# Kernel tuning notes

Hardware: AMD Instinct MI355X
Metric: run time of the kernel (lower is better)

## Reference

```python
import jax, jax.numpy as jnp
import numpy as np

N_WIRES = 4
N_OPS = 20  # depth * 10
DIM = 2 ** N_WIRES

_CNOT4 = jnp.array([[1, 0, 0, 0],
                    [0, 1, 0, 0],
                    [0, 0, 0, 1],
                    [0, 0, 1, 0]], dtype=jnp.complex64)


def _ry(t):
    c, s = jnp.cos(t / 2), jnp.sin(t / 2)
    return jnp.stack([jnp.stack([c, -s], -1), jnp.stack([s, c], -1)], -2).astype(jnp.complex64)


def _rx(t):
    c = jnp.cos(t / 2).astype(jnp.complex64)
    s = (-1j) * jnp.sin(t / 2).astype(jnp.complex64)
    return jnp.stack([jnp.stack([c, s], -1), jnp.stack([s, c], -1)], -2)


def _rz(t):
    e = jnp.exp(-0.5j * t.astype(jnp.complex64))
    z = jnp.zeros_like(e)
    return jnp.stack([jnp.stack([e, z], -1), jnp.stack([z, jnp.conj(e)], -1)], -2)


def _apply_1q(state, U, w):
    # state: [B, 2^n]; U: [2,2] (shared) or [B,2,2] (per-batch angle)
    b = state.shape[0]
    left, right = 2 ** w, 2 ** (N_WIRES - w - 1)
    s = state.reshape(b, left, 2, right)
    if U.ndim == 2:
        s = jnp.einsum('ij,bajc->baic', U, s)
    else:
        s = jnp.einsum('bij,bajc->baic', U, s)
    return s.reshape(b, -1)


def _apply_cnot(state, c):
    # CNOT on adjacent wires (c, c+1)
    b = state.shape[0]
    left, right = 2 ** c, 2 ** (N_WIRES - c - 2)
    s = state.reshape(b, left, 4, right)
    s = jnp.einsum('ij,bajc->baic', _CNOT4, s)
    return s.reshape(b, -1)


def _circuit(x, y, theta):
    b = x.shape[0]
    state = jnp.zeros((b, DIM), jnp.complex64).at[:, 0].set(1.0)
    # encoder: Ry(x_w) on each wire
    for w in range(N_WIRES):
        state = _apply_1q(state, _ry(x[:, w]), w)
    # fixed pseudo-random layer of 20 gates (RX/RY/RZ rotations + CNOTs)
    rot = (_rx, _ry, _rz)
    for i in range(N_OPS):
        kind = i % 4
        if kind == 3:
            state = _apply_cnot(state, (i // 4) % (N_WIRES - 1))
        else:
            w = (7 * i + 3) % N_WIRES
            state = _apply_1q(state, rot[kind](theta[i]), w)
    # second encoder: Ry(-y_w)
    for w in range(N_WIRES):
        state = _apply_1q(state, _ry(-y[:, w]), w)
    # PauliZ expectation on wire 0, then abs (original: abs(measure(...)[0]))
    probs = state.real ** 2 + state.imag ** 2  # [B, 16]
    p = probs.reshape(b, 2, -1)
    z0 = jnp.sum(p[:, 0], -1) - jnp.sum(p[:, 1], -1)
    return jnp.abs(z0)


def setup_inputs() -> dict:
    key = jax.random.key(0)
    k1, k2, k3 = jax.random.split(key, 3)
    B = 262144
    x = jax.random.normal(k1, (B, N_WIRES), jnp.float32)
    y = jax.random.normal(k2, (B, N_WIRES), jnp.float32)
    theta = jax.random.normal(k3, (N_OPS,), jnp.float32)
    return {"x": x, "y": y, "theta": theta}


def reference(x, y, theta):
    return _circuit(x, y, theta)
```

## Files before the change

kernel.cpp:

```cpp
#include <hip/hip_runtime.h>
#include <hip/hip_bf16.h>
#include <math.h>


template<int BIT>
__device__ __forceinline__ void rx8(float (&sr)[8], float (&si)[8], float c, float s) {
    #pragma unroll
    for (int i = 0; i < 8; ++i) {
        if (!(i & (1 << BIT))) {
            const int j = i | (1 << BIT);
            float ar = sr[i], ai = si[i], br = sr[j], bi = si[j];
            sr[i] = c * ar + s * bi;  si[i] = c * ai - s * br;
            sr[j] = c * br + s * ai;  si[j] = c * bi - s * ar;
        }
    }
}

template<int BIT>
__device__ __forceinline__ void ry8(float (&sr)[8], float (&si)[8], float c, float s) {
    #pragma unroll
    for (int i = 0; i < 8; ++i) {
        if (!(i & (1 << BIT))) {
            const int j = i | (1 << BIT);
            float ar = sr[i], ai = si[i], br = sr[j], bi = si[j];
            sr[i] = c * ar - s * br;  si[i] = c * ai - s * bi;
            sr[j] = s * ar + c * br;  si[j] = s * ai + c * bi;
        }
    }
}

template<int BIT>
__device__ __forceinline__ void rz8(float (&sr)[8], float (&si)[8], float c, float s) {
    #pragma unroll
    for (int i = 0; i < 8; ++i) {
        if (!(i & (1 << BIT))) {
            const int j = i | (1 << BIT);
            float ar = sr[i], ai = si[i], br = sr[j], bi = si[j];
            sr[i] = c * ar + s * ai;  si[i] = c * ai - s * ar;
            sr[j] = c * br - s * bi;  si[j] = c * bi + s * br;
        }
    }
}

template<int CB, int TB>
__device__ __forceinline__ void cnot8(float (&sr)[8], float (&si)[8]) {
    #pragma unroll
    for (int i = 0; i < 8; ++i) {
        if ((i & (1 << CB)) && !(i & (1 << TB))) {
            const int j = i | (1 << TB);
            float t;
            t = sr[i]; sr[i] = sr[j]; sr[j] = t;
            t = si[i]; si[i] = si[j]; si[j] = t;
        }
    }
}

__device__ __forceinline__ void tri_transform(volatile float* T, int base, int s) {
    float x0 = T[base], x1 = T[base + s], x2 = T[base + 2 * s];
    T[base]         = 0.5f * (x0 + x2);
    T[base + s]     = 0.5f * (x0 - x2);
    T[base + 2 * s] = 0.5f * x1;
}

__global__ __launch_bounds__(256) void qfused_kernel(
        const float* __restrict__ x,
        const float* __restrict__ y,
        const float* __restrict__ theta,
        float* __restrict__ out,
        int B) {
    __shared__ float Vr[2][8][8], Vi[2][8][8];
    __shared__ float Nm[64];
    __shared__ float T[27];

    const int t = threadIdx.x;
    const int b = blockIdx.x * 256 + t;
    const int bc = (b < B) ? b : (B - 1);

    const float4 xv = reinterpret_cast<const float4*>(x)[bc];
    const float  y0 = y[4 * bc];

    float tC[12], tS[12];
    #pragma unroll
    for (int i = 0; i < 12; ++i) {
        const int idx = i + (i / 3);
        const float th = 0.5f * theta[idx];
        tC[i] = __cosf(th);
        tS[i] = __sinf(th);
    }

    if (t < 16) {
        const int col = t & 7, blk = t >> 3;
        const int c0 = col & 1, c1 = (col >> 1) & 1, c2 = (col >> 2) & 1;
        float sr[8], si[8];
        #pragma unroll
        for (int i = 0; i < 8; ++i) { sr[i] = 0.0f; si[i] = 0.0f; }
        {
            const float pr = tC[2];
            const float pi = c2 ? tS[2] : -tS[2];
            const int r2s = (c2 ^ blk) << 2;
            #pragma unroll
            for (int r1 = 0; r1 < 2; ++r1) {
                const float g = (r1 == c1) ? tC[1] : (r1 ? tS[1] : -tS[1]);
                #pragma unroll
                for (int r0 = 0; r0 < 2; ++r0) {
                    const int r = r2s | (r1 << 1) | r0;
                    if (r0 == c0) { sr[r] = pr * g * tC[0]; si[r] = pi * g * tC[0]; }
                    else          { sr[r] = pi * g * tS[0]; si[r] = -pr * g * tS[0]; }
                }
            }
        }
        rx8<0>(sr, si, tC[3], tS[3]);
        ry8<1>(sr, si, tC[4], tS[4]);
        rz8<2>(sr, si, tC[5], tS[5]);
        cnot8<2, 1>(sr, si);
        rx8<0>(sr, si, tC[6], tS[6]);
        ry8<1>(sr, si, tC[7], tS[7]);
        rz8<2>(sr, si, tC[8], tS[8]);
        cnot8<1, 0>(sr, si);
        rx8<0>(sr, si, tC[9], tS[9]);
        ry8<1>(sr, si, tC[10], tS[10]);
        rz8<2>(sr, si, tC[11], tS[11]);
        const int rxr = blk << 2;
        #pragma unroll
        for (int k = 0; k < 8; ++k) {
            Vr[blk][k ^ rxr][col] = sr[k];
            Vi[blk][k ^ rxr][col] = si[k];
        }
    }
    __syncthreads();

    if (t < 64) {
        const int i = t >> 3, j = t & 7;
        float a = 0.0f;
        #pragma unroll
        for (int k = 0; k < 8; ++k) {
            a = fmaf(Vr[0][k][i], Vr[1][k][j], a);
            a = fmaf(Vi[0][k][i], Vi[1][k][j], a);
        }
        Nm[t] = a;
    }
    __syncthreads();

    if (t < 27) {
        const int d1 = t / 9, d2 = (t / 3) % 3, d3 = t % 3;
        const int ones = ((d1 == 1) << 2) | ((d2 == 1) << 1) | (d3 == 1);
        const int twos = ((d1 == 2) << 2) | ((d2 == 2) << 1) | (d3 == 2);
        float a = 0.0f;
        #pragma unroll
        for (int c = 0; c < 8; ++c) {
            if (c & ~ones) continue;
            a += Nm[(twos | c) * 8 + (twos | (ones & ~c))];
        }
        T[t] = a;
    }
    __syncthreads();

    if (t < 9) tri_transform(T, t, 9);
    __syncthreads();
    if (t < 9) tri_transform(T, 9 * (t / 3) + (t % 3), 3);
    __syncthreads();
    if (t < 9) tri_transform(T, 3 * t, 1);
    __syncthreads();

    if (b >= B) return;

    const float cx0 = __cosf(xv.x), sx0 = __sinf(xv.x);
    const float cx1 = __cosf(xv.y), sx1 = __sinf(xv.y);
    const float cx2 = __cosf(xv.z), sx2 = __sinf(xv.z);
    const float cx3 = __cosf(xv.w), sx3 = __sinf(xv.w);
    const float cy  = __cosf(y0),   sy  = __sinf(y0);

    float r3[9];
    #pragma unroll
    for (int m = 0; m < 9; ++m)
        r3[m] = fmaf(sx3, T[3 * m + 2], fmaf(cx3, T[3 * m + 1], T[3 * m]));
    float r2[3];
    #pragma unroll
    for (int m = 0; m < 3; ++m)
        r2[m] = fmaf(sx2, r3[3 * m + 2], fmaf(cx2, r3[3 * m + 1], r3[3 * m]));
    const float g = fmaf(sx1, r2[2], fmaf(cx1, r2[1], r2[0]));

    out[b] = fabsf(fmaf(cy, cx0, sy * sx0 * g));
}

extern "C" void kernel_launch(void* const* d_in, const int* in_sizes, int n_in,
                              void* d_out, int out_size, void* d_ws, size_t ws_size,
                              hipStream_t stream) {
    const float* x     = (const float*)d_in[0];
    const float* y     = (const float*)d_in[1];
    const float* theta = (const float*)d_in[2];
    float* out = (float*)d_out;

    int B = out_size;
    int block = 256;
    int grid = (B + block - 1) / block;
    qfused_kernel<<<grid, block, 0, stream>>>(x, y, theta, out, B);
}
```

Before: 11.24 us.

## Replace block-wide barriers with per-wavefront redundant setup and wave-level syncs

Each 64-lane wavefront now builds its own copy of the theta-dependent tables in private shared-memory slices, so the five __syncthreads barriers become lgkmcnt waits plus scheduling barriers. The goal is to stop three idle wavefronts from waiting on the first one during setup. In exchange the setup work is repeated four times per block. Bounds checks are removed and the grid becomes B/256, which assumes B is a multiple of 256. Relying on implicit lockstep within a wavefront for shared-memory visibility is fragile.

```diff
diff --git a/kernel.cpp b/kernel.cpp
--- a/kernel.cpp
+++ b/kernel.cpp
@@ -55,12 +55,17 @@
     }
 }
 
-__device__ __forceinline__ void tri_transform(volatile float* T, int base, int s) {
+__device__ __forceinline__ void tri_transform(float* T, int base, int s) {
     float x0 = T[base], x1 = T[base + s], x2 = T[base + 2 * s];
     T[base]         = 0.5f * (x0 + x2);
     T[base + s]     = 0.5f * (x0 - x2);
     T[base + 2 * s] = 0.5f * x1;
 }
+
+#define WAVE_SYNC() do { \
+    asm volatile("s_waitcnt lgkmcnt(0)" ::: "memory"); \
+    __builtin_amdgcn_sched_barrier(0); \
+} while (0)
 
 __global__ __launch_bounds__(256) void qfused_kernel(
         const float* __restrict__ x,
@@ -68,36 +73,35 @@
         const float* __restrict__ theta,
         float* __restrict__ out,
         int B) {
-    __shared__ float Vr[2][8][8], Vi[2][8][8];
-    __shared__ float Nm[64];
-    __shared__ float T[27];
-
-    const int t = threadIdx.x;
-    const int b = blockIdx.x * 256 + t;
-    const int bc = (b < B) ? b : (B - 1);
-
-    const float4 xv = reinterpret_cast<const float4*>(x)[bc];
-    const float  y0 = y[4 * bc];
-
-    float tC[12], tS[12];
-    #pragma unroll
-    for (int i = 0; i < 12; ++i) {
-        const int idx = i + (i / 3);
-        const float th = 0.5f * theta[idx];
-        tC[i] = __cosf(th);
-        tS[i] = __sinf(th);
-    }
-
-    if (t < 16) {
-        const int col = t & 7, blk = t >> 3;
+    __shared__ float Vr[4][2][8][8], Vi[4][2][8][8];
+    __shared__ float Nm[4][64];
+    __shared__ float T[4][27];
+
+    const int t    = threadIdx.x;
+    const int wid  = t >> 6;
+    const int lane = t & 63;
+    const int b    = blockIdx.x * 256 + t;
+
+    const float4 xv = reinterpret_cast<const float4*>(x)[b];
+    const float  y0 = y[4 * b];
+
+    if (lane < 16) {
+        float tC[12], tS[12];
+        #pragma unroll
+        for (int i = 0; i < 12; ++i) {
+            const int idx = i + (i / 3);
+            __sincosf(0.5f * theta[idx], &tS[i], &tC[i]);
+        }
+        const int col = lane & 7, blk = lane >> 3;
         const int c0 = col & 1, c1 = (col >> 1) & 1, c2 = (col >> 2) & 1;
         float sr[8], si[8];
-        #pragma unroll
-        for (int i = 0; i < 8; ++i) { sr[i] = 0.0f; si[i] = 0.0f; }
         {
             const float pr = tC[2];
             const float pi = c2 ? tS[2] : -tS[2];
             const int r2s = (c2 ^ blk) << 2;
+            const int r2o = r2s ^ 4;
+            #pragma unroll
+            for (int i = 0; i < 8; ++i) { sr[i] = 0.0f; si[i] = 0.0f; }
             #pragma unroll
             for (int r1 = 0; r1 < 2; ++r1) {
                 const float g = (r1 == c1) ? tC[1] : (r1 ? tS[1] : -tS[1]);
@@ -108,6 +112,7 @@
                     else          { sr[r] = pi * g * tS[0]; si[r] = -pr * g * tS[0]; }
                 }
             }
+            (void)r2o;
         }
         rx8<0>(sr, si, tC[3], tS[3]);
         ry8<1>(sr, si, tC[4], tS[4]);
@@ -123,46 +128,44 @@
         const int rxr = blk << 2;
         #pragma unroll
         for (int k = 0; k < 8; ++k) {
-            Vr[blk][k ^ rxr][col] = sr[k];
-            Vi[blk][k ^ rxr][col] = si[k];
-        }
-    }
-    __syncthreads();
-
-    if (t < 64) {
-        const int i = t >> 3, j = t & 7;
+            Vr[wid][blk][k ^ rxr][col] = sr[k];
+            Vi[wid][blk][k ^ rxr][col] = si[k];
+        }
+    }
+    WAVE_SYNC();
+
+    {
+        const int i = lane >> 3, j = lane & 7;
         float a = 0.0f;
         #pragma unroll
         for (int k = 0; k < 8; ++k) {
-            a = fmaf(Vr[0][k][i], Vr[1][k][j], a);
-            a = fmaf(Vi[0][k][i], Vi[1][k][j], a);
-        }
-        Nm[t] = a;
-    }
-    __syncthreads();
-
-    if (t < 27) {
-        const int d1 = t / 9, d2 = (t / 3) % 3, d3 = t % 3;
+            a = fmaf(Vr[wid][0][k][i], Vr[wid][1][k][j], a);
+            a = fmaf(Vi[wid][0][k][i], Vi[wid][1][k][j], a);
+        }
+        Nm[wid][lane] = a;
+    }
+    WAVE_SYNC();
+
+    if (lane < 27) {
+        const int d1 = lane / 9, d2 = (lane / 3) % 3, d3 = lane % 3;
         const int ones = ((d1 == 1) << 2) | ((d2 == 1) << 1) | (d3 == 1);
         const int twos = ((d1 == 2) << 2) | ((d2 == 2) << 1) | (d3 == 2);
         float a = 0.0f;
         #pragma unroll
         for (int c = 0; c < 8; ++c) {
             if (c & ~ones) continue;
-            a += Nm[(twos | c) * 8 + (twos | (ones & ~c))];
-        }
-        T[t] = a;
-    }
-    __syncthreads();
-
-    if (t < 9) tri_transform(T, t, 9);
-    __syncthreads();
-    if (t < 9) tri_transform(T, 9 * (t / 3) + (t % 3), 3);
-    __syncthreads();
-    if (t < 9) tri_transform(T, 3 * t, 1);
-    __syncthreads();
-
-    if (b >= B) return;
+            a += Nm[wid][(twos | c) * 8 + (twos | (ones & ~c))];
+        }
+        T[wid][lane] = a;
+    }
+    WAVE_SYNC();
+
+    if (lane < 9) tri_transform(&T[wid][0], lane, 9);
+    WAVE_SYNC();
+    if (lane < 9) tri_transform(&T[wid][0], 9 * (lane / 3) + (lane % 3), 3);
+    WAVE_SYNC();
+    if (lane < 9) tri_transform(&T[wid][0], 3 * lane, 1);
+    WAVE_SYNC();
 
     const float cx0 = __cosf(xv.x), sx0 = __sinf(xv.x);
     const float cx1 = __cosf(xv.y), sx1 = __sinf(xv.y);
@@ -170,10 +173,11 @@
     const float cx3 = __cosf(xv.w), sx3 = __sinf(xv.w);
     const float cy  = __cosf(y0),   sy  = __sinf(y0);
 
+    const float* Tw = &T[wid][0];
     float r3[9];
     #pragma unroll
     for (int m = 0; m < 9; ++m)
-        r3[m] = fmaf(sx3, T[3 * m + 2], fmaf(cx3, T[3 * m + 1], T[3 * m]));
+        r3[m] = fmaf(sx3, Tw[3 * m + 2], fmaf(cx3, Tw[3 * m + 1], Tw[3 * m]));
     float r2[3];
     #pragma unroll
     for (int m = 0; m < 3; ++m)
@@ -193,6 +197,6 @@
 
     int B = out_size;
     int block = 256;
-    int grid = (B + block - 1) / block;
+    int grid = B / block;
     qfused_kernel<<<grid, block, 0, stream>>>(x, y, theta, out, B);
 }
```

New measurement: 11.49 us. 1.02x slower.
